# Kernel optimization log

Hardware: AMD Instinct MI355X
Metric: run time of the kernel (lower is better)

## Reference

```python
import jax, jax.numpy as jnp
import numpy as np

D_MODEL = 768
NUM_HEADS = 12
DEPTH = D_MODEL // NUM_HEADS
LN_EPS = 1e-5


def setup_inputs() -> dict:
    key = jax.random.key(0)
    ks = jax.random.split(key, 5)
    B, S = 2, 2048
    scale = 1.0 / np.sqrt(D_MODEL)
    return {
        "Q": jax.random.normal(ks[0], (B, S, D_MODEL), jnp.float32),
        "W_q": jax.random.normal(ks[1], (D_MODEL, D_MODEL), jnp.float32) * scale,
        "b_q": jnp.zeros((D_MODEL,), jnp.float32),
        "W_k": jax.random.normal(ks[2], (D_MODEL, D_MODEL), jnp.float32) * scale,
        "b_k": jnp.zeros((D_MODEL,), jnp.float32),
        "W_v": jax.random.normal(ks[3], (D_MODEL, D_MODEL), jnp.float32) * scale,
        "b_v": jnp.zeros((D_MODEL,), jnp.float32),
        "W_o": jax.random.normal(ks[4], (D_MODEL, D_MODEL), jnp.float32) * scale,
        "b_o": jnp.zeros((D_MODEL,), jnp.float32),
        "ln_gamma": jnp.ones((D_MODEL,), jnp.float32),
        "ln_beta": jnp.zeros((D_MODEL,), jnp.float32),
    }


def _split_heads(x, B):
    # [B, S, D] -> [B, H, S, depth]
    return x.reshape(B, -1, NUM_HEADS, DEPTH).transpose(0, 2, 1, 3)


def reference(Q, W_q, b_q, W_k, b_k, W_v, b_v, W_o, b_o, ln_gamma, ln_beta):
    B = Q.shape[0]
    residual = Q
    # torch Linear: x @ W.T + b
    q = _split_heads(Q @ W_q.T + b_q, B)  # [B,H,S,dh]
    k = _split_heads(Q @ W_k.T + b_k, B)
    v = _split_heads(Q @ W_v.T + b_v, B)
    scores = jnp.einsum("bhqd,bhkd->bhqk", q, k) / jnp.sqrt(jnp.float32(DEPTH))
    attn = jax.nn.softmax(scores, axis=-1)
    out = jnp.einsum("bhqk,bhkd->bhqd", attn, v)
    out = out.transpose(0, 2, 1, 3).reshape(B, -1, D_MODEL)
    out = out @ W_o.T + b_o
    x = out + residual
    mu = jnp.mean(x, axis=-1, keepdims=True)
    var = jnp.mean(jnp.square(x - mu), axis=-1, keepdims=True)
    return (x - mu) * jax.lax.rsqrt(var + LN_EPS) * ln_gamma + ln_beta
```

## Files before the change

### kernel.cpp

```cpp
#include <hip/hip_runtime.h>
#include <hip/hip_bf16.h>

#define D_MODEL 768
#define S_LEN   2048
#define BATCH   2
#define NHEAD   12
#define DH      64
#define NTOK    (BATCH * S_LEN)

typedef __attribute__((ext_vector_type(8))) short bf16x8;
typedef __attribute__((ext_vector_type(4))) float f32x4;

__device__ inline unsigned short f2bf(float f) {
    union { float f; unsigned u; } v; v.f = f;
    unsigned u = v.u;
    u += 0x7fffu + ((u >> 16) & 1u);
    return (unsigned short)(u >> 16);
}

__device__ inline unsigned pack_bf2(float a, float b) {
    union { __hip_bfloat162 h2; unsigned u; } cv;
    cv.h2 = __float22bfloat162_rn(make_float2(a, b));
    return cv.u;
}

__device__ inline void stage16(const void* g, void* l) {
    __builtin_amdgcn_global_load_lds(
        (const __attribute__((address_space(1))) unsigned*)g,
        (__attribute__((address_space(3))) unsigned*)l, 16, 0, 0);
}

__global__ __launch_bounds__(256) void convert_kernel(
    const float* __restrict__ Q,
    const float* __restrict__ Wq, const float* __restrict__ Wk,
    const float* __restrict__ Wv, const float* __restrict__ Wo,
    unsigned short* __restrict__ Xb,
    unsigned short* __restrict__ Wqb, unsigned short* __restrict__ Wkb,
    unsigned short* __restrict__ Wvb, unsigned short* __restrict__ Wob)
{
    const int XV = NTOK * D_MODEL / 4;
    const int WV = D_MODEL * D_MODEL / 4;
    int idx = blockIdx.x * 256 + threadIdx.x;
    if (idx >= XV + 4 * WV) return;

    const float* src; unsigned short* dst; int off;
    if (idx < XV) { src = Q; dst = Xb; off = idx; }
    else {
        int i2 = idx - XV;
        int seg = i2 / WV; off = i2 - seg * WV;
        if      (seg == 0) { src = Wq; dst = Wqb; }
        else if (seg == 1) { src = Wk; dst = Wkb; }
        else if (seg == 2) { src = Wv; dst = Wvb; }
        else               { src = Wo; dst = Wob; }
    }
    float4 v = reinterpret_cast<const float4*>(src)[off];
    uint2 o;
    o.x = pack_bf2(v.x, v.y);
    o.y = pack_bf2(v.z, v.w);
    reinterpret_cast<uint2*>(dst)[off] = o;
}

#define STAGE_TILE(glob, rowstrideB, row0, k0, ldsbase, nIss)                 \
    _Pragma("unroll")                                                          \
    for (int i = 0; i < (nIss); ++i) {                                         \
        int L = i * 4096 + wv * 1024 + lane * 16;                              \
        int row = L >> 7;                                                      \
        int colb = (L & 127) ^ ((row & 7) << 4);                               \
        stage16((const char*)(glob) + (size_t)((row0) + row) * (rowstrideB)    \
                    + ((k0) << 1) + colb,                                      \
                (char*)(ldsbase) + i * 4096 + wv * 1024);                      \
    }

__global__ __launch_bounds__(256) void qkv_gemm_kernel(
    const unsigned short* __restrict__ Xb,
    const unsigned short* __restrict__ Wall,
    const float* __restrict__ bq, const float* __restrict__ bk,
    const float* __restrict__ bv,
    unsigned short* __restrict__ qb, unsigned short* __restrict__ kb,
    unsigned short* __restrict__ vtb)
{
    const int lane = threadIdx.x & 63;
    const int wv   = threadIdx.x >> 6;
    const int lr   = lane & 15;
    const int lg   = lane >> 4;
    const int row0g = blockIdx.y * 128;
    const int col0g = blockIdx.x * 64;

    __shared__ __align__(16) unsigned short At[2][128 * 64];
    __shared__ __align__(16) unsigned short Bt[2][64 * 64];

    f32x4 acc[2][4] = {};

    STAGE_TILE(Xb,   1536, row0g, 0, At[0], 4);
    STAGE_TILE(Wall, 1536, col0g, 0, Bt[0], 2);
    __syncthreads();

    for (int s = 0; s < 12; ++s) {
        int cur = s & 1;
        if (s < 11) {
            STAGE_TILE(Xb,   1536, row0g, (s + 1) * 64, At[cur ^ 1], 4);
            STAGE_TILE(Wall, 1536, col0g, (s + 1) * 64, Bt[cur ^ 1], 2);
        }
        bf16x8 a[2][2], b[4][2];
#pragma unroll
        for (int m = 0; m < 2; ++m) {
            int row = wv * 32 + m * 16 + lr, sw = (row & 7) << 4;
#pragma unroll
            for (int ks = 0; ks < 2; ++ks)
                a[m][ks] = *reinterpret_cast<const bf16x8*>(
                    (const char*)At[cur] + row * 128 + ((ks * 64 + lg * 16) ^ sw));
        }
#pragma unroll
        for (int n = 0; n < 4; ++n) {
            int row = n * 16 + lr, sw = (row & 7) << 4;
#pragma unroll
            for (int ks = 0; ks < 2; ++ks)
                b[n][ks] = *reinterpret_cast<const bf16x8*>(
                    (const char*)Bt[cur] + row * 128 + ((ks * 64 + lg * 16) ^ sw));
        }
#pragma unroll
        for (int ks = 0; ks < 2; ++ks)
#pragma unroll
            for (int m = 0; m < 2; ++m)
#pragma unroll
                for (int n = 0; n < 4; ++n)
                    acc[m][n] = __builtin_amdgcn_mfma_f32_16x16x32_bf16(
                        a[m][ks], b[n][ks], acc[m][n], 0, 0, 0);
        __syncthreads();
    }

    const int which   = blockIdx.x / 12;
    const int colbase = (blockIdx.x % 12) * 64;
    const float* bias = (which == 0) ? bq : (which == 1) ? bk : bv;
#pragma unroll
    for (int m = 0; m < 2; ++m) {
#pragma unroll
        for (int n = 0; n < 4; ++n) {
            int col = colbase + n * 16 + lr;
            float bval = bias[col];
            int h = col >> 6, d = col & 63;
            int rowg = row0g + wv * 32 + m * 16 + lg * 4;
            int bb = rowg >> 11, s0 = rowg & 2047;
            if (which == 2) {
                uint2 w;
                w.x = pack_bf2(acc[m][n][0] + bval, acc[m][n][1] + bval);
                w.y = pack_bf2(acc[m][n][2] + bval, acc[m][n][3] + bval);
                *reinterpret_cast<uint2*>(
                    vtb + ((size_t)(bb * NHEAD + h) * DH + d) * S_LEN + s0) = w;
            } else {
                unsigned short* dst = (which == 0) ? qb : kb;
#pragma unroll
                for (int r = 0; r < 4; ++r)
                    dst[((size_t)(bb * NHEAD + h) * S_LEN + s0 + r) * DH + d] =
                        f2bf(acc[m][n][r] + bval);
            }
        }
    }
}

__global__ __launch_bounds__(256) void attn_kernel(
    const unsigned short* __restrict__ qb, const unsigned short* __restrict__ kb,
    const unsigned short* __restrict__ vtb,
    unsigned short* __restrict__ attnb)
{
    const int lane = threadIdx.x & 63;
    const int wv   = threadIdx.x >> 6;
    const int lr   = lane & 15;
    const int lg   = lane >> 4;
    const int bh   = blockIdx.y;
    const int h    = bh % NHEAD, bb = bh / NHEAD;
    const int q0   = blockIdx.x * 64 + wv * 16;

    __shared__ __align__(16) unsigned short Kt[2][64 * 64];
    __shared__ __align__(16) unsigned short Vt[2][64 * 64];
    __shared__ __align__(16) unsigned short PL[4][16][68];

    const char* kbase = (const char*)(kb  + (size_t)bh * S_LEN * DH);
    const char* vbase = (const char*)(vtb + (size_t)bh * DH * S_LEN);
    const unsigned short* qptr = qb + ((size_t)bh * S_LEN + q0) * DH;

    bf16x8 bq0 = *reinterpret_cast<const bf16x8*>(qptr + (size_t)lr * DH + lg * 8);
    bf16x8 bq1 = *reinterpret_cast<const bf16x8*>(qptr + (size_t)lr * DH + 32 + lg * 8);

    float m = -1e30f, l = 0.f;
    f32x4 acc[4] = {};
    const float SC = 0.125f * 1.44269504088896f;

#pragma unroll
    for (int i = 0; i < 2; ++i) {
        int L = i * 4096 + wv * 1024 + lane * 16;
        int row = L >> 7, colb = (L & 127) ^ ((row & 7) << 4);
        stage16(kbase + (size_t)row * 128 + colb, (char*)Kt[0] + i * 4096 + wv * 1024);
        stage16(vbase + (size_t)row * 4096 + colb, (char*)Vt[0] + i * 4096 + wv * 1024);
    }
    __syncthreads();

    for (int ci = 0; ci < 32; ++ci) {
        const int cur = ci & 1;
        if (ci < 31) {
            int c1 = (ci + 1) * 64;
#pragma unroll
            for (int i = 0; i < 2; ++i) {
                int L = i * 4096 + wv * 1024 + lane * 16;
                int row = L >> 7, colb = (L & 127) ^ ((row & 7) << 4);
                stage16(kbase + (size_t)(c1 + row) * 128 + colb,
                        (char*)Kt[cur ^ 1] + i * 4096 + wv * 1024);
                stage16(vbase + (size_t)row * 4096 + (c1 << 1) + colb,
                        (char*)Vt[cur ^ 1] + i * 4096 + wv * 1024);
            }
        }

        f32x4 s[4] = {};
#pragma unroll
        for (int kt = 0; kt < 4; ++kt) {
            int row = kt * 16 + lr, sw = (row & 7) << 4;
            bf16x8 ak0 = *reinterpret_cast<const bf16x8*>(
                (const char*)Kt[cur] + row * 128 + ((lg * 16) ^ sw));
            bf16x8 ak1 = *reinterpret_cast<const bf16x8*>(
                (const char*)Kt[cur] + row * 128 + ((64 + lg * 16) ^ sw));
            s[kt] = __builtin_amdgcn_mfma_f32_16x16x32_bf16(ak0, bq0, s[kt], 0, 0, 0);
            s[kt] = __builtin_amdgcn_mfma_f32_16x16x32_bf16(ak1, bq1, s[kt], 0, 0, 0);
        }

        bf16x8 av0[4], av1[4];
#pragma unroll
        for (int t = 0; t < 4; ++t) {
            int row = t * 16 + lr, sw = (row & 7) << 4;
            av0[t] = *reinterpret_cast<const bf16x8*>(
                (const char*)Vt[cur] + row * 128 + ((lg * 16) ^ sw));
            av1[t] = *reinterpret_cast<const bf16x8*>(
                (const char*)Vt[cur] + row * 128 + ((64 + lg * 16) ^ sw));
        }

        float p[16];
#pragma unroll
        for (int kt = 0; kt < 4; ++kt)
#pragma unroll
            for (int r = 0; r < 4; ++r) p[kt * 4 + r] = s[kt][r] * SC;

        float mx = fmaxf(fmaxf(fmaxf(p[0], p[1]), fmaxf(p[2], p[3])),
                         fmaxf(fmaxf(p[4], p[5]), fmaxf(p[6], p[7])));
        mx = fmaxf(mx, fmaxf(fmaxf(fmaxf(p[8], p[9]), fmaxf(p[10], p[11])),
                             fmaxf(fmaxf(p[12], p[13]), fmaxf(p[14], p[15]))));
        mx = fmaxf(mx, __shfl_xor(mx, 16));
        mx = fmaxf(mx, __shfl_xor(mx, 32));
        float mn = fmaxf(m, mx);

        float sum = 0.f;
#pragma unroll
        for (int j = 0; j < 16; ++j) {
            p[j] = __builtin_amdgcn_exp2f(p[j] - mn);
            sum += p[j];
        }
        sum += __shfl_xor(sum, 16);
        sum += __shfl_xor(sum, 32);
        float sf = __builtin_amdgcn_exp2f(m - mn);
        l = l * sf + sum; m = mn;
#pragma unroll
        for (int t = 0; t < 4; ++t) acc[t] *= sf;

#pragma unroll
        for (int kt = 0; kt < 4; ++kt) {
            uint2 w;
            w.x = pack_bf2(p[kt * 4 + 0], p[kt * 4 + 1]);
            w.y = pack_bf2(p[kt * 4 + 2], p[kt * 4 + 3]);
            *reinterpret_cast<uint2*>(&PL[wv][lr][kt * 16 + lg * 4]) = w;
        }
        union { bf16x8 v; uint2 u[2]; } bp0, bp1;
        bp0.u[0] = *reinterpret_cast<const uint2*>(&PL[wv][lr][lg * 8]);
        bp0.u[1] = *reinterpret_cast<const uint2*>(&PL[wv][lr][lg * 8 + 4]);
        bp1.u[0] = *reinterpret_cast<const uint2*>(&PL[wv][lr][32 + lg * 8]);
        bp1.u[1] = *reinterpret_cast<const uint2*>(&PL[wv][lr][32 + lg * 8 + 4]);

#pragma unroll
        for (int t = 0; t < 4; ++t) {
            acc[t] = __builtin_amdgcn_mfma_f32_16x16x32_bf16(av0[t], bp0.v, acc[t], 0, 0, 0);
            acc[t] = __builtin_amdgcn_mfma_f32_16x16x32_bf16(av1[t], bp1.v, acc[t], 0, 0, 0);
        }
        __syncthreads();
    }

    float rl = 1.0f / l;
    size_t rowbase = ((size_t)(bb * S_LEN + q0 + lr)) * D_MODEL + h * DH;
#pragma unroll
    for (int t = 0; t < 4; ++t) {
        unsigned w0 = pack_bf2(acc[t][0] * rl, acc[t][1] * rl);
        unsigned w1 = pack_bf2(acc[t][2] * rl, acc[t][3] * rl);
        *reinterpret_cast<unsigned*>(attnb + rowbase + t * 16 + lg * 4)     = w0;
        *reinterpret_cast<unsigned*>(attnb + rowbase + t * 16 + lg * 4 + 2) = w1;
    }
}

__global__ __launch_bounds__(256) void oproj_kernel(
    const unsigned short* __restrict__ attnb, const unsigned short* __restrict__ Wob,
    const float* __restrict__ bo, const float* __restrict__ Qres,
    float* __restrict__ Y)
{
    const int lane = threadIdx.x & 63;
    const int wv   = threadIdx.x >> 6;
    const int lr   = lane & 15;
    const int lg   = lane >> 4;
    const int row0g = blockIdx.y * 128;
    const int col0g = blockIdx.x * 64;

    __shared__ __align__(16) unsigned short At[2][128 * 64];
    __shared__ __align__(16) unsigned short Bt[2][64 * 64];

    f32x4 acc[2][4] = {};

    STAGE_TILE(attnb, 1536, row0g, 0, At[0], 4);
    STAGE_TILE(Wob,   1536, col0g, 0, Bt[0], 2);
    __syncthreads();

    for (int s = 0; s < 12; ++s) {
        int cur = s & 1;
        if (s < 11) {
            STAGE_TILE(attnb, 1536, row0g, (s + 1) * 64, At[cur ^ 1], 4);
            STAGE_TILE(Wob,   1536, col0g, (s + 1) * 64, Bt[cur ^ 1], 2);
        }
        bf16x8 a[2][2], b[4][2];
#pragma unroll
        for (int m = 0; m < 2; ++m) {
            int row = wv * 32 + m * 16 + lr, sw = (row & 7) << 4;
#pragma unroll
            for (int ks = 0; ks < 2; ++ks)
                a[m][ks] = *reinterpret_cast<const bf16x8*>(
                    (const char*)At[cur] + row * 128 + ((ks * 64 + lg * 16) ^ sw));
        }
#pragma unroll
        for (int n = 0; n < 4; ++n) {
            int row = n * 16 + lr, sw = (row & 7) << 4;
#pragma unroll
            for (int ks = 0; ks < 2; ++ks)
                b[n][ks] = *reinterpret_cast<const bf16x8*>(
                    (const char*)Bt[cur] + row * 128 + ((ks * 64 + lg * 16) ^ sw));
        }
#pragma unroll
        for (int ks = 0; ks < 2; ++ks)
#pragma unroll
            for (int m = 0; m < 2; ++m)
#pragma unroll
                for (int n = 0; n < 4; ++n)
                    acc[m][n] = __builtin_amdgcn_mfma_f32_16x16x32_bf16(
                        a[m][ks], b[n][ks], acc[m][n], 0, 0, 0);
        __syncthreads();
    }

#pragma unroll
    for (int m = 0; m < 2; ++m)
#pragma unroll
        for (int n = 0; n < 4; ++n) {
            int col = col0g + n * 16 + lr;
            float bval = bo[col];
#pragma unroll
            for (int r = 0; r < 4; ++r) {
                int row = row0g + wv * 32 + m * 16 + lg * 4 + r;
                size_t off = (size_t)row * D_MODEL + col;
                Y[off] = acc[m][n][r] + bval + Qres[off];
            }
        }
}

__global__ __launch_bounds__(256) void ln_kernel(
    const float* __restrict__ Y,
    const float* __restrict__ gamma, const float* __restrict__ beta,
    float* __restrict__ out)
{
    const int lane = threadIdx.x & 63;
    const int row  = blockIdx.x * 4 + (threadIdx.x >> 6);
    const float4* yr = reinterpret_cast<const float4*>(Y + (size_t)row * D_MODEL);

    float4 v[3];
    float sum = 0.f, ss = 0.f;
#pragma unroll
    for (int j = 0; j < 3; ++j) {
        v[j] = yr[lane + 64 * j];
        sum += v[j].x + v[j].y + v[j].z + v[j].w;
        ss  += v[j].x * v[j].x + v[j].y * v[j].y + v[j].z * v[j].z + v[j].w * v[j].w;
    }
#pragma unroll
    for (int msk = 1; msk < 64; msk <<= 1) {
        sum += __shfl_xor(sum, msk);
        ss  += __shfl_xor(ss,  msk);
    }
    float mu  = sum * (1.f / 768.f);
    float var = ss * (1.f / 768.f) - mu * mu;
    float is  = rsqrtf(var + 1e-5f);

    const float4* g4 = reinterpret_cast<const float4*>(gamma);
    const float4* b4 = reinterpret_cast<const float4*>(beta);
    float4* o4 = reinterpret_cast<float4*>(out + (size_t)row * D_MODEL);
#pragma unroll
    for (int j = 0; j < 3; ++j) {
        float4 g = g4[lane + 64 * j], b = b4[lane + 64 * j], r;
        r.x = (v[j].x - mu) * is * g.x + b.x;
        r.y = (v[j].y - mu) * is * g.y + b.y;
        r.z = (v[j].z - mu) * is * g.z + b.z;
        r.w = (v[j].w - mu) * is * g.w + b.w;
        o4[lane + 64 * j] = r;
    }
}

extern "C" void kernel_launch(void* const* d_in, const int* in_sizes, int n_in,
                              void* d_out, int out_size, void* d_ws, size_t ws_size,
                              hipStream_t stream)
{
    const float* Q     = (const float*)d_in[0];
    const float* Wq    = (const float*)d_in[1];
    const float* bq    = (const float*)d_in[2];
    const float* Wk    = (const float*)d_in[3];
    const float* bk    = (const float*)d_in[4];
    const float* Wv    = (const float*)d_in[5];
    const float* bv    = (const float*)d_in[6];
    const float* Wo    = (const float*)d_in[7];
    const float* bo    = (const float*)d_in[8];
    const float* gamma = (const float*)d_in[9];
    const float* beta  = (const float*)d_in[10];
    float* out = (float*)d_out;

    char* ws = (char*)d_ws;
    unsigned short* Xb    = (unsigned short*)(ws + 0);
    unsigned short* Wqb   = (unsigned short*)(ws + 6291456);
    unsigned short* Wkb   = (unsigned short*)(ws + 7471104);
    unsigned short* Wvb   = (unsigned short*)(ws + 8650752);
    unsigned short* Wob   = (unsigned short*)(ws + 9830400);
    unsigned short* qb    = (unsigned short*)(ws + 11010048);
    unsigned short* kb    = (unsigned short*)(ws + 17301504);
    unsigned short* vtb   = (unsigned short*)(ws + 23592960);
    unsigned short* attnb = (unsigned short*)(ws + 29884416);
    float*          Yf    = (float*)        (ws + 36175872);

    convert_kernel<<<5376, 256, 0, stream>>>(Q, Wq, Wk, Wv, Wo, Xb, Wqb, Wkb, Wvb, Wob);
    qkv_gemm_kernel<<<dim3(36, 32), 256, 0, stream>>>(Xb, Wqb, bq, bk, bv, qb, kb, vtb);
    attn_kernel<<<dim3(32, 24), 256, 0, stream>>>(qb, kb, vtb, attnb);
    oproj_kernel<<<dim3(12, 32), 256, 0, stream>>>(attnb, Wob, bo, Q, Yf);
    ln_kernel<<<1024, 256, 0, stream>>>(Yf, gamma, beta, out);
}
```

Measured before the change: 117.8 us.

## Streamline attention inner loop with lazy rescale, precomputed addresses, and priority hints

Rewrites the flash-attention chunk loop as a macro unrolled by two with precomputed LDS and global pointers, so per-iteration address arithmetic drops out. It adds a lazy online-softmax rescale that only updates the running max when it grows by more than 8 in log2 units, folds the scale into the exp2 argument with an fma, and changes the P buffer from padded to XOR-swizzled. It also raises wave priority around the MFMA blocks. The lazy max means unnormalised exponents can reach up to 2^8, which is a numerical risk with bf16 P values.

After: 110.9 us. 5.8% less time.

```diff
diff --git a/kernel.cpp b/kernel.cpp
--- a/kernel.cpp
+++ b/kernel.cpp
@@ -158,6 +158,78 @@
     }
 }
 
+#define ATTN_CHUNK(P, CI)                                                      \
+    {                                                                          \
+        if ((CI) < 31) {                                                       \
+            stage16(kg0, sdK[(P) ^ 1]);                                        \
+            stage16(kg1, sdK[(P) ^ 1] + 4096);                                 \
+            stage16(vg0, sdV[(P) ^ 1]);                                        \
+            stage16(vg1, sdV[(P) ^ 1] + 4096);                                 \
+            kg0 += 8192; kg1 += 8192; vg0 += 128; vg1 += 128;                  \
+        }                                                                      \
+        f32x4 s[4] = {};                                                       \
+        __builtin_amdgcn_s_setprio(1);                                         \
+        _Pragma("unroll")                                                      \
+        for (int kt = 0; kt < 4; ++kt) {                                       \
+            bf16x8 ak0 = *(const bf16x8*)(rdK[P] + kt * 2048);                 \
+            bf16x8 ak1 = *(const bf16x8*)(rdK[P] + kt * 2048 + oD);            \
+            s[kt] = __builtin_amdgcn_mfma_f32_16x16x32_bf16(ak0, bq0, s[kt], 0, 0, 0); \
+            s[kt] = __builtin_amdgcn_mfma_f32_16x16x32_bf16(ak1, bq1, s[kt], 0, 0, 0); \
+        }                                                                      \
+        __builtin_amdgcn_s_setprio(0);                                         \
+        bf16x8 av0[4], av1[4];                                                 \
+        _Pragma("unroll")                                                      \
+        for (int t = 0; t < 4; ++t) {                                          \
+            av0[t] = *(const bf16x8*)(rdV[P] + t * 2048);                      \
+            av1[t] = *(const bf16x8*)(rdV[P] + t * 2048 + oD);                 \
+        }                                                                      \
+        float mxr = fmaxf(fmaxf(fmaxf(s[0][0], s[0][1]), fmaxf(s[0][2], s[0][3])), \
+                          fmaxf(fmaxf(s[1][0], s[1][1]), fmaxf(s[1][2], s[1][3]))); \
+        mxr = fmaxf(mxr, fmaxf(fmaxf(fmaxf(s[2][0], s[2][1]), fmaxf(s[2][2], s[2][3])), \
+                               fmaxf(fmaxf(s[3][0], s[3][1]), fmaxf(s[3][2], s[3][3])))); \
+        mxr = fmaxf(mxr, __shfl_xor(mxr, 16));                                 \
+        mxr = fmaxf(mxr, __shfl_xor(mxr, 32));                                 \
+        float mxs = mxr * SC;                                                  \
+        if (__any(mxs > m + 8.0f)) {                                           \
+            float mn = fmaxf(m, mxs);                                          \
+            float sf = __builtin_amdgcn_exp2f(m - mn);                         \
+            m = mn; l *= sf;                                                   \
+            _Pragma("unroll")                                                  \
+            for (int t = 0; t < 4; ++t) acc[t] *= sf;                          \
+        }                                                                      \
+        float p[16];                                                           \
+        _Pragma("unroll")                                                      \
+        for (int kt = 0; kt < 4; ++kt)                                         \
+            _Pragma("unroll")                                                  \
+            for (int r = 0; r < 4; ++r)                                        \
+                p[kt * 4 + r] = __builtin_amdgcn_exp2f(fmaf(s[kt][r], SC, -m)); \
+        float sum = ((p[0] + p[1]) + (p[2] + p[3])) + ((p[4] + p[5]) + (p[6] + p[7])); \
+        sum += ((p[8] + p[9]) + (p[10] + p[11])) + ((p[12] + p[13]) + (p[14] + p[15])); \
+        sum += __shfl_xor(sum, 16);                                            \
+        sum += __shfl_xor(sum, 32);                                            \
+        l += sum;                                                              \
+        _Pragma("unroll")                                                      \
+        for (int kt = 0; kt < 4; ++kt) {                                       \
+            uint2 w;                                                           \
+            w.x = pack_bf2(p[kt * 4 + 0], p[kt * 4 + 1]);                      \
+            w.y = pack_bf2(p[kt * 4 + 2], p[kt * 4 + 3]);                      \
+            *(uint2*)(plw + ((kt * 32 + lg * 8) ^ swr)) = w;                   \
+        }                                                                      \
+        union { bf16x8 v; uint2 u[2]; } bp0, bp1;                              \
+        bp0.u[0] = *(const uint2*)(plr);                                       \
+        bp0.u[1] = *(const uint2*)(plr + 8);                                   \
+        bp1.u[0] = *(const uint2*)(plr + oD);                                  \
+        bp1.u[1] = *(const uint2*)(plr + oD + 8);                              \
+        __builtin_amdgcn_s_setprio(1);                                         \
+        _Pragma("unroll")                                                      \
+        for (int t = 0; t < 4; ++t) {                                          \
+            acc[t] = __builtin_amdgcn_mfma_f32_16x16x32_bf16(av0[t], bp0.v, acc[t], 0, 0, 0); \
+            acc[t] = __builtin_amdgcn_mfma_f32_16x16x32_bf16(av1[t], bp1.v, acc[t], 0, 0, 0); \
+        }                                                                      \
+        __builtin_amdgcn_s_setprio(0);                                         \
+        __syncthreads();                                                       \
+    }
+
 __global__ __launch_bounds__(256) void attn_kernel(
     const unsigned short* __restrict__ qb, const unsigned short* __restrict__ kb,
     const unsigned short* __restrict__ vtb,
@@ -173,7 +245,7 @@
 
     __shared__ __align__(16) unsigned short Kt[2][64 * 64];
     __shared__ __align__(16) unsigned short Vt[2][64 * 64];
-    __shared__ __align__(16) unsigned short PL[4][16][68];
+    __shared__ __align__(16) unsigned short PL[4][16][64];
 
     const char* kbase = (const char*)(kb  + (size_t)bh * S_LEN * DH);
     const char* vbase = (const char*)(vtb + (size_t)bh * DH * S_LEN);
@@ -182,102 +254,41 @@
     bf16x8 bq0 = *reinterpret_cast<const bf16x8*>(qptr + (size_t)lr * DH + lg * 8);
     bf16x8 bq1 = *reinterpret_cast<const bf16x8*>(qptr + (size_t)lr * DH + 32 + lg * 8);
 
+    const int swr = (lr & 7) << 4;
+    const int o0  = (lg * 16) ^ swr;
+    const int oD  = (o0 ^ 64) - o0;
+    const int L1  = wv * 1024 + lane * 16;
+    const int r1  = L1 >> 7;
+    const int cb1 = (L1 & 127) ^ ((r1 & 7) << 4);
+
+    const char* kg0 = kbase + (size_t)r1 * 128 + cb1;
+    const char* kg1 = kbase + (size_t)(32 + r1) * 128 + cb1;
+    const char* vg0 = vbase + (size_t)r1 * 4096 + cb1;
+    const char* vg1 = vbase + (size_t)(32 + r1) * 4096 + cb1;
+
+    char* sdK[2] = { (char*)Kt[0] + wv * 1024, (char*)Kt[1] + wv * 1024 };
+    char* sdV[2] = { (char*)Vt[0] + wv * 1024, (char*)Vt[1] + wv * 1024 };
+    const char* rdK[2] = {
+        (const char*)Kt[0] + lr * 128 + o0,
+        (const char*)Kt[1] + lr * 128 + o0 };
+    const char* rdV[2] = {
+        (const char*)Vt[0] + lr * 128 + o0,
+        (const char*)Vt[1] + lr * 128 + o0 };
+    char* plw = (char*)PL + wv * 2048 + lr * 128;
+    const char* plr = plw + o0;
+
     float m = -1e30f, l = 0.f;
     f32x4 acc[4] = {};
     const float SC = 0.125f * 1.44269504088896f;
 
-#pragma unroll
-    for (int i = 0; i < 2; ++i) {
-        int L = i * 4096 + wv * 1024 + lane * 16;
-        int row = L >> 7, colb = (L & 127) ^ ((row & 7) << 4);
-        stage16(kbase + (size_t)row * 128 + colb, (char*)Kt[0] + i * 4096 + wv * 1024);
-        stage16(vbase + (size_t)row * 4096 + colb, (char*)Vt[0] + i * 4096 + wv * 1024);
-    }
+    stage16(kg0, sdK[0]); stage16(kg1, sdK[0] + 4096);
+    stage16(vg0, sdV[0]); stage16(vg1, sdV[0] + 4096);
+    kg0 += 8192; kg1 += 8192; vg0 += 128; vg1 += 128;
     __syncthreads();
 
-    for (int ci = 0; ci < 32; ++ci) {
-        const int cur = ci & 1;
-        if (ci < 31) {
-            int c1 = (ci + 1) * 64;
-#pragma unroll
-            for (int i = 0; i < 2; ++i) {
-                int L = i * 4096 + wv * 1024 + lane * 16;
-                int row = L >> 7, colb = (L & 127) ^ ((row & 7) << 4);
-                stage16(kbase + (size_t)(c1 + row) * 128 + colb,
-                        (char*)Kt[cur ^ 1] + i * 4096 + wv * 1024);
-                stage16(vbase + (size_t)row * 4096 + (c1 << 1) + colb,
-                        (char*)Vt[cur ^ 1] + i * 4096 + wv * 1024);
-            }
-        }
-
-        f32x4 s[4] = {};
-#pragma unroll
-        for (int kt = 0; kt < 4; ++kt) {
-            int row = kt * 16 + lr, sw = (row & 7) << 4;
-            bf16x8 ak0 = *reinterpret_cast<const bf16x8*>(
-                (const char*)Kt[cur] + row * 128 + ((lg * 16) ^ sw));
-            bf16x8 ak1 = *reinterpret_cast<const bf16x8*>(
-                (const char*)Kt[cur] + row * 128 + ((64 + lg * 16) ^ sw));
-            s[kt] = __builtin_amdgcn_mfma_f32_16x16x32_bf16(ak0, bq0, s[kt], 0, 0, 0);
-            s[kt] = __builtin_amdgcn_mfma_f32_16x16x32_bf16(ak1, bq1, s[kt], 0, 0, 0);
-        }
-
-        bf16x8 av0[4], av1[4];
-#pragma unroll
-        for (int t = 0; t < 4; ++t) {
-            int row = t * 16 + lr, sw = (row & 7) << 4;
-            av0[t] = *reinterpret_cast<const bf16x8*>(
-                (const char*)Vt[cur] + row * 128 + ((lg * 16) ^ sw));
-            av1[t] = *reinterpret_cast<const bf16x8*>(
-                (const char*)Vt[cur] + row * 128 + ((64 + lg * 16) ^ sw));
-        }
-
-        float p[16];
-#pragma unroll
-        for (int kt = 0; kt < 4; ++kt)
-#pragma unroll
-            for (int r = 0; r < 4; ++r) p[kt * 4 + r] = s[kt][r] * SC;
-
-        float mx = fmaxf(fmaxf(fmaxf(p[0], p[1]), fmaxf(p[2], p[3])),
-                         fmaxf(fmaxf(p[4], p[5]), fmaxf(p[6], p[7])));
-        mx = fmaxf(mx, fmaxf(fmaxf(fmaxf(p[8], p[9]), fmaxf(p[10], p[11])),
-                             fmaxf(fmaxf(p[12], p[13]), fmaxf(p[14], p[15]))));
-        mx = fmaxf(mx, __shfl_xor(mx, 16));
-        mx = fmaxf(mx, __shfl_xor(mx, 32));
-        float mn = fmaxf(m, mx);
-
-        float sum = 0.f;
-#pragma unroll
-        for (int j = 0; j < 16; ++j) {
-            p[j] = __builtin_amdgcn_exp2f(p[j] - mn);
-            sum += p[j];
-        }
-        sum += __shfl_xor(sum, 16);
-        sum += __shfl_xor(sum, 32);
-        float sf = __builtin_amdgcn_exp2f(m - mn);
-        l = l * sf + sum; m = mn;
-#pragma unroll
-        for (int t = 0; t < 4; ++t) acc[t] *= sf;
-
-#pragma unroll
-        for (int kt = 0; kt < 4; ++kt) {
-            uint2 w;
-            w.x = pack_bf2(p[kt * 4 + 0], p[kt * 4 + 1]);
-            w.y = pack_bf2(p[kt * 4 + 2], p[kt * 4 + 3]);
-            *reinterpret_cast<uint2*>(&PL[wv][lr][kt * 16 + lg * 4]) = w;
-        }
-        union { bf16x8 v; uint2 u[2]; } bp0, bp1;
-        bp0.u[0] = *reinterpret_cast<const uint2*>(&PL[wv][lr][lg * 8]);
-        bp0.u[1] = *reinterpret_cast<const uint2*>(&PL[wv][lr][lg * 8 + 4]);
-        bp1.u[0] = *reinterpret_cast<const uint2*>(&PL[wv][lr][32 + lg * 8]);
-        bp1.u[1] = *reinterpret_cast<const uint2*>(&PL[wv][lr][32 + lg * 8 + 4]);
-
-#pragma unroll
-        for (int t = 0; t < 4; ++t) {
-            acc[t] = __builtin_amdgcn_mfma_f32_16x16x32_bf16(av0[t], bp0.v, acc[t], 0, 0, 0);
-            acc[t] = __builtin_amdgcn_mfma_f32_16x16x32_bf16(av1[t], bp1.v, acc[t], 0, 0, 0);
-        }
-        __syncthreads();
+    for (int it = 0; it < 16; ++it) {
+        ATTN_CHUNK(0, it * 2);
+        ATTN_CHUNK(1, it * 2 + 1);
     }
 
     float rl = 1.0f / l;
```
